# Performance work log

Hardware: AMD Instinct MI355X
Metric: run time of the kernel (lower is better)

Reference implementation:

```python
import jax, jax.numpy as jnp
import numpy as np

VOCAB = 1024
ENC_D = 256
PRED_D = 256
JOINT_D = ENC_D + PRED_D


def setup_inputs() -> dict:
    key = jax.random.key(0)
    k1, k2, k3, k4, k5, k6 = jax.random.split(key, 6)
    B, T, U = 8, 256, 64
    encoder_outputs = jax.random.normal(k1, (B, T, ENC_D), dtype=jnp.float32)
    decoder_outputs = jax.random.normal(k2, (B, U, PRED_D), dtype=jnp.float32)
    s1 = 1.0 / np.sqrt(JOINT_D)
    W1 = jax.random.uniform(k3, (JOINT_D, JOINT_D), dtype=jnp.float32, minval=-s1, maxval=s1)
    b1 = jax.random.uniform(k4, (JOINT_D,), dtype=jnp.float32, minval=-s1, maxval=s1)
    W2 = jax.random.uniform(k5, (VOCAB, JOINT_D), dtype=jnp.float32, minval=-s1, maxval=s1)
    b2 = jax.random.uniform(k6, (VOCAB,), dtype=jnp.float32, minval=-s1, maxval=s1)
    return {"encoder_outputs": encoder_outputs, "decoder_outputs": decoder_outputs,
            "W1": W1, "b1": b1, "W2": W2, "b2": b2}


def reference(encoder_outputs, decoder_outputs, W1, b1, W2, b2):
    # Decompose the first linear over the concat: split W1 into enc/dec blocks,
    # project each sequence separately, then broadcast-add over (t, u).
    # This is the same math as cat([enc_rep, dec_rep], -1) @ W1.T + b1.
    W1e = W1[:, :ENC_D]   # [J, E]
    W1d = W1[:, ENC_D:]   # [J, P]
    enc_proj = jnp.einsum('bte,je->btj', encoder_outputs, W1e)  # [B,T,J]
    dec_proj = jnp.einsum('bup,jp->buj', decoder_outputs, W1d)  # [B,U,J]
    h = enc_proj[:, :, None, :] + dec_proj[:, None, :, :] + b1  # [B,T,U,J]
    h = jnp.tanh(h)
    logits = jnp.einsum('btuj,vj->btuv', h, W2) + b2             # [B,T,U,V]
    return jax.nn.log_softmax(logits, axis=-1)
```

## Files before the change

kernel.cpp:

```cpp
#include <hip/hip_runtime.h>
#include <hip/hip_bf16.h>
#include <cstdint>
#include <cstddef>

#define NB 8
#define NT 256
#define NU 64
#define DJ 512
#define DV 1024
#define DK 256

typedef __attribute__((ext_vector_type(8))) short short8;
typedef __attribute__((ext_vector_type(4))) float floatx4;

__device__ __forceinline__ unsigned short f2bf(float x) {
    unsigned int u = __float_as_uint(x);
    u += 0x7fffu + ((u >> 16) & 1u);
    return (unsigned short)(u >> 16);
}

__global__ __launch_bounds__(256) void stage1_gemm(
    const float* __restrict__ enc, const float* __restrict__ dec,
    const float* __restrict__ W1, const float* __restrict__ b1,
    float* __restrict__ enc_proj, float* __restrict__ dec_proj)
{
    __shared__ float As[64][17];
    __shared__ float Bs[16][65];

    const int n0 = blockIdx.x * 64;
    const int m0 = blockIdx.y * 64;
    const bool is_enc = (m0 < NB * NT);
    const float* A = is_enc ? enc : dec;
    const int arow0 = is_enc ? m0 : (m0 - NB * NT);
    const int koff  = is_enc ? 0 : DK;
    float* C = is_enc ? enc_proj : dec_proj;

    const int tid = threadIdx.x;
    const int kk = tid & 15;
    const int grp = tid >> 4;
    const int tx = tid & 15;
    const int ty = tid >> 4;

    float acc[4][4] = {};

    for (int k0 = 0; k0 < DK; k0 += 16) {
        #pragma unroll
        for (int g = 0; g < 4; g++) {
            As[grp + g * 16][kk] = A[(size_t)(arow0 + grp + g * 16) * DK + k0 + kk];
            Bs[kk][grp + g * 16] = W1[(size_t)(n0 + grp + g * 16) * DJ + koff + k0 + kk];
        }
        __syncthreads();
        #pragma unroll
        for (int k = 0; k < 16; k++) {
            float av[4], bv[4];
            #pragma unroll
            for (int i = 0; i < 4; i++) av[i] = As[ty * 4 + i][k];
            #pragma unroll
            for (int j = 0; j < 4; j++) bv[j] = Bs[k][tx * 4 + j];
            #pragma unroll
            for (int i = 0; i < 4; i++)
                #pragma unroll
                for (int j = 0; j < 4; j++)
                    acc[i][j] = fmaf(av[i], bv[j], acc[i][j]);
        }
        __syncthreads();
    }

    float4 bias = make_float4(0.f, 0.f, 0.f, 0.f);
    if (is_enc) bias = *(const float4*)&b1[n0 + tx * 4];
    #pragma unroll
    for (int i = 0; i < 4; i++) {
        const int row = arow0 + ty * 4 + i;
        float4 v;
        v.x = acc[i][0] + bias.x;
        v.y = acc[i][1] + bias.y;
        v.z = acc[i][2] + bias.z;
        v.w = acc[i][3] + bias.w;
        *(float4*)&C[(size_t)row * DJ + n0 + tx * 4] = v;
    }
}

__global__ __launch_bounds__(256) void convert_w2(
    const float* __restrict__ W2, unsigned short* __restrict__ W2b)
{
    const int i = (blockIdx.x * 256 + threadIdx.x) * 4;
    float4 v = *(const float4*)(W2 + i);
    ushort4 o;
    o.x = f2bf(v.x); o.y = f2bf(v.y); o.z = f2bf(v.z); o.w = f2bf(v.w);
    *(ushort4*)(W2b + i) = o;
}

__global__ __launch_bounds__(512, 4) void joint_kernel(
    const float* __restrict__ enc_proj, const float* __restrict__ dec_proj,
    const unsigned short* __restrict__ W2b, const float* __restrict__ b2,
    float* __restrict__ out)
{
    __shared__ __align__(16) unsigned char smem[32768];
    unsigned short* ha = (unsigned short*)smem;

    const int bt = blockIdx.x;
    const int uh = blockIdx.y;
    const int b = bt >> 8;
    const int tid = threadIdx.x;

    {
        const int j0 = (tid & 127) * 4;
        const int ug = tid >> 7;
        const float4 e = *(const float4*)(enc_proj + (size_t)bt * DJ + j0);
        const float* dp = dec_proj + (size_t)(b * NU + uh * 32 + ug * 8) * DJ + j0;
        const int chunk = j0 >> 3;
        const int wi = j0 & 7;
        #pragma unroll
        for (int i = 0; i < 8; i++) {
            const int u = ug * 8 + i;
            float4 d = *(const float4*)(dp + (size_t)i * DJ);
            float x0 = e.x + d.x, x1 = e.y + d.y, x2 = e.z + d.z, x3 = e.w + d.w;
            ushort4 o;
            o.x = f2bf(1.f - 2.f / (__expf(2.f * x0) + 1.f));
            o.y = f2bf(1.f - 2.f / (__expf(2.f * x1) + 1.f));
            o.z = f2bf(1.f - 2.f / (__expf(2.f * x2) + 1.f));
            o.w = f2bf(1.f - 2.f / (__expf(2.f * x3) + 1.f));
            *(ushort4*)(ha + (size_t)u * DJ + (((chunk ^ (u & 7)) << 3) + wi)) = o;
        }
    }
    __syncthreads();

    const int w = tid >> 6;
    const int lane = tid & 63;
    const int q = lane >> 4;
    const int nn = lane & 15;
    const int wbase = w * 128;

    floatx4 acc[2][8];
    #pragma unroll
    for (int rt = 0; rt < 2; rt++)
        #pragma unroll
        for (int ct = 0; ct < 8; ct++)
            acc[rt][ct] = (floatx4){0.f, 0.f, 0.f, 0.f};

    const unsigned short* wrow0 = W2b + (size_t)(wbase + nn * 4) * DJ;
    const unsigned short* wrow1 = W2b + (size_t)(wbase + 64 + nn * 4) * DJ;

    for (int ks = 0; ks < 16; ks++) {
        short8 av[2];
        #pragma unroll
        for (int rt = 0; rt < 2; rt++) {
            const int u = rt * 16 + nn;
            const int c = ((ks * 4 + q) ^ (u & 7)) << 3;
            av[rt] = *(const short8*)(ha + (size_t)u * DJ + c);
        }
        const int ko = ks * 32 + q * 8;
        {
            short8 bv[4];
            #pragma unroll
            for (int c4 = 0; c4 < 4; c4++)
                bv[c4] = *(const short8*)(wrow0 + (size_t)c4 * DJ + ko);
            #pragma unroll
            for (int rt = 0; rt < 2; rt++)
                #pragma unroll
                for (int c4 = 0; c4 < 4; c4++)
                    acc[rt][c4] = __builtin_amdgcn_mfma_f32_16x16x32_bf16(
                        av[rt], bv[c4], acc[rt][c4], 0, 0, 0);
        }
        {
            short8 bv[4];
            #pragma unroll
            for (int c4 = 0; c4 < 4; c4++)
                bv[c4] = *(const short8*)(wrow1 + (size_t)c4 * DJ + ko);
            #pragma unroll
            for (int rt = 0; rt < 2; rt++)
                #pragma unroll
                for (int c4 = 0; c4 < 4; c4++)
                    acc[rt][4 + c4] = __builtin_amdgcn_mfma_f32_16x16x32_bf16(
                        av[rt], bv[c4], acc[rt][4 + c4], 0, 0, 0);
        }
    }

    __syncthreads();

    float* wred     = (float*)smem;
    float* rowoff_s = (float*)(smem + 1024);

    float b2a[8];
    *(float4*)&b2a[0] = *(const float4*)(b2 + wbase + nn * 4);
    *(float4*)&b2a[4] = *(const float4*)(b2 + wbase + 64 + nn * 4);
    #pragma unroll
    for (int rt = 0; rt < 2; rt++)
        #pragma unroll
        for (int ct = 0; ct < 8; ct++)
            #pragma unroll
            for (int r = 0; r < 4; r++)
                acc[rt][ct][r] += b2a[ct];

    #pragma unroll
    for (int rt = 0; rt < 2; rt++) {
        #pragma unroll
        for (int r = 0; r < 4; r++) {
            float s = 0.f;
            #pragma unroll
            for (int ct = 0; ct < 8; ct++) s += __expf(acc[rt][ct][r]);
            #pragma unroll
            for (int mk = 1; mk <= 8; mk <<= 1) s += __shfl_xor(s, mk, 64);
            if (nn == 0) wred[(rt * 16 + q * 4 + r) * 8 + w] = s;
        }
    }
    __syncthreads();
    if (tid < 32) {
        float4 s0 = *(const float4*)&wred[tid * 8];
        float4 s1 = *(const float4*)&wred[tid * 8 + 4];
        float s = ((s0.x + s0.y) + (s0.z + s0.w)) + ((s1.x + s1.y) + (s1.z + s1.w));
        rowoff_s[tid] = __logf(s);
    }
    __syncthreads();

    float* outb = out + ((size_t)bt * NU + (size_t)uh * 32) * DV;
    #pragma unroll
    for (int rt = 0; rt < 2; rt++) {
        #pragma unroll
        for (int r = 0; r < 4; r++) {
            const int u = rt * 16 + q * 4 + r;
            const float off = rowoff_s[u];
            floatx4 v0, v1;
            v0[0] = acc[rt][0][r] - off; v0[1] = acc[rt][1][r] - off;
            v0[2] = acc[rt][2][r] - off; v0[3] = acc[rt][3][r] - off;
            v1[0] = acc[rt][4][r] - off; v1[1] = acc[rt][5][r] - off;
            v1[2] = acc[rt][6][r] - off; v1[3] = acc[rt][7][r] - off;
            __builtin_nontemporal_store(v0, (floatx4*)(outb + (size_t)u * DV + wbase + nn * 4));
            __builtin_nontemporal_store(v1, (floatx4*)(outb + (size_t)u * DV + wbase + 64 + nn * 4));
        }
    }
}

extern "C" void kernel_launch(void* const* d_in, const int* in_sizes, int n_in,
                              void* d_out, int out_size, void* d_ws, size_t ws_size,
                              hipStream_t stream) {
    const float* enc = (const float*)d_in[0];
    const float* dec = (const float*)d_in[1];
    const float* W1  = (const float*)d_in[2];
    const float* b1  = (const float*)d_in[3];
    const float* W2  = (const float*)d_in[4];
    const float* b2  = (const float*)d_in[5];
    float* out = (float*)d_out;

    float* enc_proj = (float*)d_ws;
    float* dec_proj = enc_proj + (size_t)(NB * NT) * DJ;
    unsigned short* W2b = (unsigned short*)(dec_proj + (size_t)DJ * DJ);

    dim3 g1(8, 40);
    stage1_gemm<<<g1, 256, 0, stream>>>(enc, dec, W1, b1, enc_proj, dec_proj);
    convert_w2<<<512, 256, 0, stream>>>(W2, W2b);
    dim3 gj(NB * NT, 2);
    joint_kernel<<<gj, 512, 0, stream>>>(enc_proj, dec_proj, W2b, b2, out);
}
```

Before: 955.4 us.

## Process all 64 u rows per block and double-buffer W2 fragment loads

Each joint block now covers all 64 decoder positions for one (b,t) instead of 32, doubling the M tile. Every W2 fragment loaded from global/L2 is reused across twice as many MFMAs, and the grid shrinks by half. The K loop is unrolled by two with register double-buffering of the B fragments to hide load latency. In exchange LDS doubles to 64KB, accumulators double to 128 floats per thread, and launch bounds drop to 2 blocks per CU, which lowers occupancy and adds register pressure.

```diff
diff --git a/kernel.cpp b/kernel.cpp
--- a/kernel.cpp
+++ b/kernel.cpp
@@ -90,16 +90,15 @@
     *(ushort4*)(W2b + i) = o;
 }
 
-__global__ __launch_bounds__(512, 4) void joint_kernel(
+__global__ __launch_bounds__(512, 2) void joint_kernel(
     const float* __restrict__ enc_proj, const float* __restrict__ dec_proj,
     const unsigned short* __restrict__ W2b, const float* __restrict__ b2,
     float* __restrict__ out)
 {
-    __shared__ __align__(16) unsigned char smem[32768];
+    __shared__ __align__(16) unsigned char smem[65536];
     unsigned short* ha = (unsigned short*)smem;
 
     const int bt = blockIdx.x;
-    const int uh = blockIdx.y;
     const int b = bt >> 8;
     const int tid = threadIdx.x;
 
@@ -107,12 +106,12 @@
         const int j0 = (tid & 127) * 4;
         const int ug = tid >> 7;
         const float4 e = *(const float4*)(enc_proj + (size_t)bt * DJ + j0);
-        const float* dp = dec_proj + (size_t)(b * NU + uh * 32 + ug * 8) * DJ + j0;
+        const float* dp = dec_proj + (size_t)(b * NU + ug * 16) * DJ + j0;
         const int chunk = j0 >> 3;
         const int wi = j0 & 7;
-        #pragma unroll
-        for (int i = 0; i < 8; i++) {
-            const int u = ug * 8 + i;
+        #pragma unroll 4
+        for (int i = 0; i < 16; i++) {
+            const int u = ug * 16 + i;
             float4 d = *(const float4*)(dp + (size_t)i * DJ);
             float x0 = e.x + d.x, x1 = e.y + d.y, x2 = e.z + d.z, x3 = e.w + d.w;
             ushort4 o;
@@ -131,61 +130,75 @@
     const int nn = lane & 15;
     const int wbase = w * 128;
 
-    floatx4 acc[2][8];
-    #pragma unroll
-    for (int rt = 0; rt < 2; rt++)
+    floatx4 acc[4][8];
+    #pragma unroll
+    for (int rt = 0; rt < 4; rt++)
         #pragma unroll
         for (int ct = 0; ct < 8; ct++)
             acc[rt][ct] = (floatx4){0.f, 0.f, 0.f, 0.f};
 
-    const unsigned short* wrow0 = W2b + (size_t)(wbase + nn * 4) * DJ;
-    const unsigned short* wrow1 = W2b + (size_t)(wbase + 64 + nn * 4) * DJ;
-
-    for (int ks = 0; ks < 16; ks++) {
-        short8 av[2];
-        #pragma unroll
-        for (int rt = 0; rt < 2; rt++) {
+    const unsigned short* pB0 = W2b + (size_t)(wbase + nn * 4) * DJ + q * 8;
+    const unsigned short* pB1 = pB0 + (size_t)64 * DJ;
+
+    short8 bv0[8], bv1[8];
+    short8 av[4];
+
+    #pragma unroll
+    for (int c4 = 0; c4 < 4; c4++) {
+        bv0[c4]     = *(const short8*)(pB0 + (size_t)c4 * DJ);
+        bv0[4 + c4] = *(const short8*)(pB1 + (size_t)c4 * DJ);
+    }
+
+    for (int ks = 0; ks < 16; ks += 2) {
+        #pragma unroll
+        for (int c4 = 0; c4 < 4; c4++) {
+            bv1[c4]     = *(const short8*)(pB0 + (size_t)c4 * DJ + (ks + 1) * 32);
+            bv1[4 + c4] = *(const short8*)(pB1 + (size_t)c4 * DJ + (ks + 1) * 32);
+        }
+        #pragma unroll
+        for (int rt = 0; rt < 4; rt++) {
             const int u = rt * 16 + nn;
             const int c = ((ks * 4 + q) ^ (u & 7)) << 3;
             av[rt] = *(const short8*)(ha + (size_t)u * DJ + c);
         }
-        const int ko = ks * 32 + q * 8;
-        {
-            short8 bv[4];
-            #pragma unroll
-            for (int c4 = 0; c4 < 4; c4++)
-                bv[c4] = *(const short8*)(wrow0 + (size_t)c4 * DJ + ko);
-            #pragma unroll
-            for (int rt = 0; rt < 2; rt++)
-                #pragma unroll
-                for (int c4 = 0; c4 < 4; c4++)
-                    acc[rt][c4] = __builtin_amdgcn_mfma_f32_16x16x32_bf16(
-                        av[rt], bv[c4], acc[rt][c4], 0, 0, 0);
-        }
-        {
-            short8 bv[4];
-            #pragma unroll
-            for (int c4 = 0; c4 < 4; c4++)
-                bv[c4] = *(const short8*)(wrow1 + (size_t)c4 * DJ + ko);
-            #pragma unroll
-            for (int rt = 0; rt < 2; rt++)
-                #pragma unroll
-                for (int c4 = 0; c4 < 4; c4++)
-                    acc[rt][4 + c4] = __builtin_amdgcn_mfma_f32_16x16x32_bf16(
-                        av[rt], bv[c4], acc[rt][4 + c4], 0, 0, 0);
-        }
+        #pragma unroll
+        for (int ct = 0; ct < 8; ct++)
+            #pragma unroll
+            for (int rt = 0; rt < 4; rt++)
+                acc[rt][ct] = __builtin_amdgcn_mfma_f32_16x16x32_bf16(
+                    av[rt], bv0[ct], acc[rt][ct], 0, 0, 0);
+
+        if (ks + 2 < 16) {
+            #pragma unroll
+            for (int c4 = 0; c4 < 4; c4++) {
+                bv0[c4]     = *(const short8*)(pB0 + (size_t)c4 * DJ + (ks + 2) * 32);
+                bv0[4 + c4] = *(const short8*)(pB1 + (size_t)c4 * DJ + (ks + 2) * 32);
+            }
+        }
+        #pragma unroll
+        for (int rt = 0; rt < 4; rt++) {
+            const int u = rt * 16 + nn;
+            const int c = (((ks + 1) * 4 + q) ^ (u & 7)) << 3;
+            av[rt] = *(const short8*)(ha + (size_t)u * DJ + c);
+        }
+        #pragma unroll
+        for (int ct = 0; ct < 8; ct++)
+            #pragma unroll
+            for (int rt = 0; rt < 4; rt++)
+                acc[rt][ct] = __builtin_amdgcn_mfma_f32_16x16x32_bf16(
+                    av[rt], bv1[ct], acc[rt][ct], 0, 0, 0);
     }
 
     __syncthreads();
 
     float* wred     = (float*)smem;
-    float* rowoff_s = (float*)(smem + 1024);
+    float* rowoff_s = (float*)(smem + 2048);
 
     float b2a[8];
     *(float4*)&b2a[0] = *(const float4*)(b2 + wbase + nn * 4);
     *(float4*)&b2a[4] = *(const float4*)(b2 + wbase + 64 + nn * 4);
     #pragma unroll
-    for (int rt = 0; rt < 2; rt++)
+    for (int rt = 0; rt < 4; rt++)
         #pragma unroll
         for (int ct = 0; ct < 8; ct++)
             #pragma unroll
@@ -193,7 +206,7 @@
                 acc[rt][ct][r] += b2a[ct];
 
     #pragma unroll
-    for (int rt = 0; rt < 2; rt++) {
+    for (int rt = 0; rt < 4; rt++) {
         #pragma unroll
         for (int r = 0; r < 4; r++) {
             float s = 0.f;
@@ -205,7 +218,7 @@
         }
     }
     __syncthreads();
-    if (tid < 32) {
+    if (tid < 64) {
         float4 s0 = *(const float4*)&wred[tid * 8];
         float4 s1 = *(const float4*)&wred[tid * 8 + 4];
         float s = ((s0.x + s0.y) + (s0.z + s0.w)) + ((s1.x + s1.y) + (s1.z + s1.w));
@@ -213,9 +226,9 @@
     }
     __syncthreads();
 
-    float* outb = out + ((size_t)bt * NU + (size_t)uh * 32) * DV;
-    #pragma unroll
-    for (int rt = 0; rt < 2; rt++) {
+    float* outb = out + (size_t)bt * NU * DV;
+    #pragma unroll
+    for (int rt = 0; rt < 4; rt++) {
         #pragma unroll
         for (int r = 0; r < 4; r++) {
             const int u = rt * 16 + q * 4 + r;
@@ -249,6 +262,5 @@
     dim3 g1(8, 40);
     stage1_gemm<<<g1, 256, 0, stream>>>(enc, dec, W1, b1, enc_proj, dec_proj);
     convert_w2<<<512, 256, 0, stream>>>(W2, W2b);
-    dim3 gj(NB * NT, 2);
-    joint_kernel<<<gj, 512, 0, stream>>>(enc_proj, dec_proj, W2b, b2, out);
-}
+    joint_kernel<<<NB * NT, 512, 0, stream>>>(enc_proj, dec_proj, W2b, b2, out);
+}
```

Result: faster. 836.4 us (-12.5%).
